# Kernel optimization log

Measured on AMD Instinct MI355X. Metric: run time of the kernel, lower is better.

The kernel has to match this reference:

```python
import jax, jax.numpy as jnp
import numpy as np


def dense_image_warp(image, flow):
    """Faithful port of tfa.image.dense_image_warp.
    query(y,x) = grid(y,x) - flow(y,x); bilinear sample with floor clipped to
    [0, size-2] and alpha clipped to [0,1] (matches tfa _interpolate_bilinear 'ij').
    image: [B,H,W,C] float, flow: [B,H,W,2] float -> [B,H,W,C]
    """
    B, H, W, C = image.shape
    gy = jnp.arange(H, dtype=flow.dtype)
    gx = jnp.arange(W, dtype=flow.dtype)
    grid = jnp.stack(jnp.meshgrid(gy, gx, indexing='ij'), axis=-1)  # [H,W,2]
    query = grid[None] - flow  # [B,H,W,2]
    qy, qx = query[..., 0], query[..., 1]
    fy = jnp.clip(jnp.floor(qy), 0.0, H - 2)
    fx = jnp.clip(jnp.floor(qx), 0.0, W - 2)
    ay = jnp.clip(qy - fy, 0.0, 1.0)[..., None]  # [B,H,W,1]
    ax = jnp.clip(qx - fx, 0.0, 1.0)[..., None]
    y0 = fy.astype(jnp.int32)
    x0 = fx.astype(jnp.int32)
    b = jnp.arange(B)[:, None, None]
    tl = image[b, y0, x0]
    tr = image[b, y0, x0 + 1]
    bl = image[b, y0 + 1, x0]
    br = image[b, y0 + 1, x0 + 1]
    top = tl + ax * (tr - tl)
    bot = bl + ax * (br - bl)
    return top + ay * (bot - top)


def setup_inputs() -> dict:
    key = jax.random.key(0)
    ks = jax.random.split(key, 6)
    B, H, W, C = 16, 512, 512, 3
    return {
        'frame_0': jax.random.uniform(ks[0], (B, H, W, C), jnp.float32),
        'frame_1': jax.random.uniform(ks[1], (B, H, W, C), jnp.float32),
        'f_01': jax.random.normal(ks[2], (B, H, W, 2), jnp.float32) * 5.0,
        'f_10': jax.random.normal(ks[3], (B, H, W, 2), jnp.float32) * 5.0,
        'f_t0': jax.random.normal(ks[4], (B, H, W, 2), jnp.float32) * 5.0,
        'f_t1': jax.random.normal(ks[5], (B, H, W, 2), jnp.float32) * 5.0,
    }


def reference(frame_0, frame_1, f_01, f_10, f_t0, f_t1):
    return (
        dense_image_warp(frame_1, f_01),
        dense_image_warp(frame_0, f_10),
        dense_image_warp(frame_0, f_t0),
        dense_image_warp(frame_1, f_t1),
    )
```

## Files before the change

kernel.cpp:

```cpp
#include <hip/hip_runtime.h>

#define HH 512
#define WW 512
#define NPIX (16 * HH * WW)
#define IMG_DW (HH * WW * 3)
#define ROWD_G (WW * 3)

#define TS    32
#define APR   12
#define LW    (TS + 2 * APR)
#define ROWD  (LW * 3)
#define LSTR  172
#define LDSDW (LW * LSTR)

typedef float fv4 __attribute__((ext_vector_type(4)));
typedef float fv2 __attribute__((ext_vector_type(2)));
typedef fv4 fv4u __attribute__((aligned(4)));
typedef fv2 fv2u __attribute__((aligned(4)));

__device__ __forceinline__ void sample(const float* __restrict__ imgb,
                                       const float* __restrict__ s,
                                       int AX0, int AY0,
                                       float qy, float qx, float* __restrict__ r)
{
    float fy = floorf(qy); fy = fminf(fmaxf(fy, 0.0f), (float)(HH - 2));
    float fx = floorf(qx); fx = fminf(fmaxf(fx, 0.0f), (float)(WW - 2));
    const float ay = fminf(fmaxf(qy - fy, 0.0f), 1.0f);
    const float ax = fminf(fmaxf(qx - fx, 0.0f), 1.0f);
    const int y0 = (int)fy, x0 = (int)fx;
    const int yl = y0 - AY0, xl = x0 - AX0;
    if ((unsigned)yl < (unsigned)(LW - 1) && (unsigned)xl < (unsigned)(LW - 1)) {
        const float* t  = s + yl * LSTR + 3 * xl;
        const float* bo = t + LSTR;
#pragma unroll
        for (int c = 0; c < 3; ++c) {
            const float tl = t[c],  tr = t[c + 3];
            const float bl = bo[c], br = bo[c + 3];
            const float top = tl + ax * (tr - tl);
            const float bot = bl + ax * (br - bl);
            r[c] = top + ay * (bot - top);
        }
    } else {
        const float* t  = imgb + ((size_t)y0 * WW + x0) * 3;
        const float* bo = t + WW * 3;
        const fv4u t4 = *(const fv4u*)t;  const fv2u t2 = *(const fv2u*)(t + 4);
        const fv4u b4 = *(const fv4u*)bo; const fv2u b2 = *(const fv2u*)(bo + 4);
        const float tv[6] = {t4.x, t4.y, t4.z, t4.w, t2.x, t2.y};
        const float bv[6] = {b4.x, b4.y, b4.z, b4.w, b2.x, b2.y};
#pragma unroll
        for (int c = 0; c < 3; ++c) {
            const float top = tv[c] + ax * (tv[c + 3] - tv[c]);
            const float bot = bv[c] + ax * (bv[c + 3] - bv[c]);
            r[c] = top + ay * (bot - top);
        }
    }
}

__global__ __launch_bounds__(256) void warp_glds_kernel(
    const float* __restrict__ frame0, const float* __restrict__ frame1,
    const float* __restrict__ f01, const float* __restrict__ f10,
    const float* __restrict__ ft0, const float* __restrict__ ft1,
    float* __restrict__ out)
{
    __shared__ float lds[LDSDW];

    const unsigned bid = blockIdx.x;
    const unsigned v   = (bid & 7u) * 1024u + (bid >> 3);

    const unsigned tile  = v & 255u;
    const unsigned img_b = v >> 8;
    const int b  = (int)(img_b & 15u);
    const int fg = (int)(img_b >> 4);

    const int tx = (int)(tile & 15u);
    const int ty = (int)(tile >> 4);
    const int X0 = tx * TS, Y0 = ty * TS;
    const int AX0 = X0 - APR, AY0 = Y0 - APR;

    const float* img   = fg ? frame1 : frame0;
    const float* flowA = fg ? f01 : f10;
    const float* flowB = fg ? ft1 : ft0;
    const size_t opA   = fg ? 0 : 1;
    const size_t opB   = fg ? 3 : 2;

    const float* imgb = img + (size_t)b * IMG_DW;

    const int tid = (int)threadIdx.x;
    const int lx = (tid & 7) * 4;
    const int ly = tid >> 3;
    const int x = X0 + lx, y = Y0 + ly;
    const size_t pixIn = ((size_t)b * HH + y) * WW + x;

    const fv4 a0 = __builtin_nontemporal_load((const fv4*)(flowA + pixIn * 2));
    const fv4 a1 = __builtin_nontemporal_load((const fv4*)(flowA + pixIn * 2) + 1);
    const fv4 c0 = __builtin_nontemporal_load((const fv4*)(flowB + pixIn * 2));
    const fv4 c1 = __builtin_nontemporal_load((const fv4*)(flowB + pixIn * 2) + 1);

    {
        const unsigned wid = __builtin_amdgcn_readfirstlane((unsigned)tid >> 6);
        int D   = tid * 4;
        int row = D / LSTR;
        int rd  = D - row * LSTR;
#pragma unroll
        for (int it = 0; it < 10; ++it) {
            if (tid * 4 + it * 1024 < LDSDW) {
                const int gy = min(max(AY0 + row, 0), HH - 1);
                int idx = gy * ROWD_G + AX0 * 3 + rd;
                idx = min(max(idx, 0), IMG_DW - 4);
                const float* src = imgb + idx;
                float* dst = (float*)lds + it * 1024 + wid * 256;
                __builtin_amdgcn_global_load_lds(
                    (const __attribute__((address_space(1))) void*)src,
                    (__attribute__((address_space(3))) void*)dst, 16, 0, 0);
            }
            row += 5; rd += 164;
            if (rd >= LSTR) { rd -= LSTR; ++row; }
        }
    }
    __syncthreads();

    float* oA = out + (opA * NPIX + pixIn) * 3;
    float* oB = out + (opB * NPIX + pixIn) * 3;

    {
        const float fly[4] = {a0.x, a0.z, a1.x, a1.z};
        const float flx[4] = {a0.y, a0.w, a1.y, a1.w};
        float res[12];
#pragma unroll
        for (int p = 0; p < 4; ++p)
            sample(imgb, lds, AX0, AY0, (float)y - fly[p], (float)(x + p) - flx[p], res + 3 * p);
        fv4 v0s = {res[0], res[1], res[2],  res[3]};
        fv4 v1s = {res[4], res[5], res[6],  res[7]};
        fv4 v2s = {res[8], res[9], res[10], res[11]};
        __builtin_nontemporal_store(v0s, (fv4*)oA);
        __builtin_nontemporal_store(v1s, (fv4*)oA + 1);
        __builtin_nontemporal_store(v2s, (fv4*)oA + 2);
    }
    {
        const float fly[4] = {c0.x, c0.z, c1.x, c1.z};
        const float flx[4] = {c0.y, c0.w, c1.y, c1.w};
        float res[12];
#pragma unroll
        for (int p = 0; p < 4; ++p)
            sample(imgb, lds, AX0, AY0, (float)y - fly[p], (float)(x + p) - flx[p], res + 3 * p);
        fv4 v0s = {res[0], res[1], res[2],  res[3]};
        fv4 v1s = {res[4], res[5], res[6],  res[7]};
        fv4 v2s = {res[8], res[9], res[10], res[11]};
        __builtin_nontemporal_store(v0s, (fv4*)oB);
        __builtin_nontemporal_store(v1s, (fv4*)oB + 1);
        __builtin_nontemporal_store(v2s, (fv4*)oB + 2);
    }
}

extern "C" void kernel_launch(void* const* d_in, const int* in_sizes, int n_in,
                              void* d_out, int out_size, void* d_ws, size_t ws_size,
                              hipStream_t stream) {
    const float* frame0 = (const float*)d_in[0];
    const float* frame1 = (const float*)d_in[1];
    const float* f01    = (const float*)d_in[2];
    const float* f10    = (const float*)d_in[3];
    const float* ft0    = (const float*)d_in[4];
    const float* ft1    = (const float*)d_in[5];
    float* out = (float*)d_out;

    hipLaunchKernelGGL(warp_glds_kernel, dim3(8192), dim3(256), 0, stream,
                       frame0, frame1, f01, f10, ft0, ft1, out);
}
```

Measured before the change: 103.1 us.

## Shrink tiles to 32x16 with two pixels per thread and doubled grid

Halves the tile height to 16 rows, so each thread handles two pixels instead of four and the grid doubles to 16384 blocks. The LDS apron tile shrinks to 40 rows and the cooperative global-to-LDS fill drops to 7 iterations with a tail guard. This is meant to raise parallelism and occupancy and cut per-thread latency chains. In exchange the apron overhead per output pixel grows, so more redundant image loads go into LDS, and output stores narrow to 8-byte writes.

```diff
diff --git a/kernel.cpp b/kernel.cpp
--- a/kernel.cpp
+++ b/kernel.cpp
@@ -6,12 +6,14 @@
 #define IMG_DW (HH * WW * 3)
 #define ROWD_G (WW * 3)
 
-#define TS    32
+#define TSX   32
+#define TSY   16
 #define APR   12
-#define LW    (TS + 2 * APR)
-#define ROWD  (LW * 3)
+#define LWX   (TSX + 2 * APR)
+#define LWY   (TSY + 2 * APR)
+#define ROWD  (LWX * 3)
 #define LSTR  172
-#define LDSDW (LW * LSTR)
+#define LDSDW (LWY * LSTR)
 
 typedef float fv4 __attribute__((ext_vector_type(4)));
 typedef float fv2 __attribute__((ext_vector_type(2)));
@@ -29,7 +31,7 @@
     const float ax = fminf(fmaxf(qx - fx, 0.0f), 1.0f);
     const int y0 = (int)fy, x0 = (int)fx;
     const int yl = y0 - AY0, xl = x0 - AX0;
-    if ((unsigned)yl < (unsigned)(LW - 1) && (unsigned)xl < (unsigned)(LW - 1)) {
+    if ((unsigned)yl < (unsigned)(LWY - 1) && (unsigned)xl < (unsigned)(LWX - 1)) {
         const float* t  = s + yl * LSTR + 3 * xl;
         const float* bo = t + LSTR;
 #pragma unroll
@@ -56,7 +58,7 @@
     }
 }
 
-__global__ __launch_bounds__(256) void warp_glds_kernel(
+__global__ __launch_bounds__(256) void warp_glds16_kernel(
     const float* __restrict__ frame0, const float* __restrict__ frame1,
     const float* __restrict__ f01, const float* __restrict__ f10,
     const float* __restrict__ ft0, const float* __restrict__ ft1,
@@ -65,16 +67,16 @@
     __shared__ float lds[LDSDW];
 
     const unsigned bid = blockIdx.x;
-    const unsigned v   = (bid & 7u) * 1024u + (bid >> 3);
+    const unsigned v   = (bid & 7u) * 2048u + (bid >> 3);
 
-    const unsigned tile  = v & 255u;
-    const unsigned img_b = v >> 8;
+    const unsigned tile  = v & 511u;
+    const unsigned img_b = v >> 9;
     const int b  = (int)(img_b & 15u);
     const int fg = (int)(img_b >> 4);
 
     const int tx = (int)(tile & 15u);
     const int ty = (int)(tile >> 4);
-    const int X0 = tx * TS, Y0 = ty * TS;
+    const int X0 = tx * TSX, Y0 = ty * TSY;
     const int AX0 = X0 - APR, AY0 = Y0 - APR;
 
     const float* img   = fg ? frame1 : frame0;
@@ -86,15 +88,13 @@
     const float* imgb = img + (size_t)b * IMG_DW;
 
     const int tid = (int)threadIdx.x;
-    const int lx = (tid & 7) * 4;
-    const int ly = tid >> 3;
+    const int lx = (tid & 15) * 2;
+    const int ly = tid >> 4;
     const int x = X0 + lx, y = Y0 + ly;
     const size_t pixIn = ((size_t)b * HH + y) * WW + x;
 
-    const fv4 a0 = __builtin_nontemporal_load((const fv4*)(flowA + pixIn * 2));
-    const fv4 a1 = __builtin_nontemporal_load((const fv4*)(flowA + pixIn * 2) + 1);
-    const fv4 c0 = __builtin_nontemporal_load((const fv4*)(flowB + pixIn * 2));
-    const fv4 c1 = __builtin_nontemporal_load((const fv4*)(flowB + pixIn * 2) + 1);
+    const fv4 a = __builtin_nontemporal_load((const fv4*)(flowA + pixIn * 2));
+    const fv4 c = __builtin_nontemporal_load((const fv4*)(flowB + pixIn * 2));
 
     {
         const unsigned wid = __builtin_amdgcn_readfirstlane((unsigned)tid >> 6);
@@ -102,8 +102,8 @@
         int row = D / LSTR;
         int rd  = D - row * LSTR;
 #pragma unroll
-        for (int it = 0; it < 10; ++it) {
-            if (tid * 4 + it * 1024 < LDSDW) {
+        for (int it = 0; it < 7; ++it) {
+            if (it < 6 || tid < 184) {
                 const int gy = min(max(AY0 + row, 0), HH - 1);
                 int idx = gy * ROWD_G + AX0 * 3 + rd;
                 idx = min(max(idx, 0), IMG_DW - 4);
@@ -123,32 +123,26 @@
     float* oB = out + (opB * NPIX + pixIn) * 3;
 
     {
-        const float fly[4] = {a0.x, a0.z, a1.x, a1.z};
-        const float flx[4] = {a0.y, a0.w, a1.y, a1.w};
-        float res[12];
-#pragma unroll
-        for (int p = 0; p < 4; ++p)
-            sample(imgb, lds, AX0, AY0, (float)y - fly[p], (float)(x + p) - flx[p], res + 3 * p);
-        fv4 v0s = {res[0], res[1], res[2],  res[3]};
-        fv4 v1s = {res[4], res[5], res[6],  res[7]};
-        fv4 v2s = {res[8], res[9], res[10], res[11]};
-        __builtin_nontemporal_store(v0s, (fv4*)oA);
-        __builtin_nontemporal_store(v1s, (fv4*)oA + 1);
-        __builtin_nontemporal_store(v2s, (fv4*)oA + 2);
+        float res[6];
+        sample(imgb, lds, AX0, AY0, (float)y - a.x, (float)x       - a.y, res);
+        sample(imgb, lds, AX0, AY0, (float)y - a.z, (float)(x + 1) - a.w, res + 3);
+        fv2 v0s = {res[0], res[1]};
+        fv2 v1s = {res[2], res[3]};
+        fv2 v2s = {res[4], res[5]};
+        __builtin_nontemporal_store(v0s, (fv2*)oA);
+        __builtin_nontemporal_store(v1s, (fv2*)oA + 1);
+        __builtin_nontemporal_store(v2s, (fv2*)oA + 2);
     }
     {
-        const float fly[4] = {c0.x, c0.z, c1.x, c1.z};
-        const float flx[4] = {c0.y, c0.w, c1.y, c1.w};
-        float res[12];
-#pragma unroll
-        for (int p = 0; p < 4; ++p)
-            sample(imgb, lds, AX0, AY0, (float)y - fly[p], (float)(x + p) - flx[p], res + 3 * p);
-        fv4 v0s = {res[0], res[1], res[2],  res[3]};
-        fv4 v1s = {res[4], res[5], res[6],  res[7]};
-        fv4 v2s = {res[8], res[9], res[10], res[11]};
-        __builtin_nontemporal_store(v0s, (fv4*)oB);
-        __builtin_nontemporal_store(v1s, (fv4*)oB + 1);
-        __builtin_nontemporal_store(v2s, (fv4*)oB + 2);
+        float res[6];
+        sample(imgb, lds, AX0, AY0, (float)y - c.x, (float)x       - c.y, res);
+        sample(imgb, lds, AX0, AY0, (float)y - c.z, (float)(x + 1) - c.w, res + 3);
+        fv2 v0s = {res[0], res[1]};
+        fv2 v1s = {res[2], res[3]};
+        fv2 v2s = {res[4], res[5]};
+        __builtin_nontemporal_store(v0s, (fv2*)oB);
+        __builtin_nontemporal_store(v1s, (fv2*)oB + 1);
+        __builtin_nontemporal_store(v2s, (fv2*)oB + 2);
     }
 }
 
@@ -163,6 +157,6 @@
     const float* ft1    = (const float*)d_in[5];
     float* out = (float*)d_out;
 
-    hipLaunchKernelGGL(warp_glds_kernel, dim3(8192), dim3(256), 0, stream,
+    hipLaunchKernelGGL(warp_glds16_kernel, dim3(16384), dim3(256), 0, stream,
                        frame0, frame1, f01, f10, ft0, ft1, out);
 }
```

New measurement: 94.72 us. 1.09x faster.
